# Performance work log

Measured on AMD Instinct MI355X. Metric: run time of the kernel, lower is better.

## Reference

```python
import jax, jax.numpy as jnp
import numpy as np

B, S, H = 2, 2048, 1024
NH, HD = 16, 64
WIN = 256
EPS = 1e-5


def _layernorm(x, g, b):
    # normalize over last dim (head_dim)
    m = jnp.mean(x, axis=-1, keepdims=True)
    v = jnp.mean((x - m) ** 2, axis=-1, keepdims=True)
    return (x - m) * jax.lax.rsqrt(v + EPS) * g + b


def setup_inputs() -> dict:
    key = jax.random.key(0)
    ks = jax.random.split(key, 6)
    scale = 1.0 / np.sqrt(2.0 * H)  # ~ xavier_uniform with gain 1/sqrt(2)
    inp = {
        "x": jax.random.normal(ks[0], (B, S, H), dtype=jnp.float32),
        "Wq": jax.random.normal(ks[1], (H, H), dtype=jnp.float32) * scale,
        "bq": jnp.zeros((H,), jnp.float32),
        "Wk": jax.random.normal(ks[2], (H, H), dtype=jnp.float32) * scale,
        "bk": jnp.zeros((H,), jnp.float32),
        "Wv": jax.random.normal(ks[3], (H, H), dtype=jnp.float32) * scale,
        "bv": jnp.zeros((H,), jnp.float32),
        "Wo": jax.random.normal(ks[4], (H, H), dtype=jnp.float32) * scale,
        "bo": jnp.zeros((H,), jnp.float32),
        "ln_q_w": jnp.ones((HD,), jnp.float32),
        "ln_q_b": jnp.zeros((HD,), jnp.float32),
        "ln_k_w": jnp.ones((HD,), jnp.float32),
        "ln_k_b": jnp.zeros((HD,), jnp.float32),
    }
    return inp


def reference(x, Wq, bq, Wk, bk, Wv, bv, Wo, bo, ln_q_w, ln_q_b, ln_k_w, ln_k_b):
    b, s, _ = x.shape
    # projections (torch Linear: x @ W.T + b)
    q = (x @ Wq.T + bq).reshape(b, s, NH, HD)
    k = (x @ Wk.T + bk).reshape(b, s, NH, HD)
    v = (x @ Wv.T + bv).reshape(b, s, NH, HD)
    # QK layernorm over head_dim
    q = _layernorm(q, ln_q_w, ln_q_b)
    k = _layernorm(k, ln_k_w, ln_k_b)
    # scores [b, h, s, s]
    scores = jnp.einsum("bqhd,bkhd->bhqk", q, k) / np.sqrt(HD).astype(np.float32)
    i = jnp.arange(s)[:, None]
    j = jnp.arange(s)[None, :]
    mask = (j <= i) & (i - j <= WIN)
    scores = jnp.where(mask[None, None], scores, -jnp.inf)
    probs = jax.nn.softmax(scores, axis=-1)
    out = jnp.einsum("bhqk,bkhd->bqhd", probs, v).reshape(b, s, NH * HD)
    return out @ Wo.T + bo
```

## Files before the change

### kernel.cpp

```cpp
#include <hip/hip_runtime.h>
#include <hip/hip_bf16.h>
#include <cstdint>

typedef __hip_bfloat16 bf16;
typedef __attribute__((ext_vector_type(8))) short s16x8;
typedef __attribute__((ext_vector_type(4))) float f32x4;

#define NB_B 2
#define NB_S 2048
#define NB_H 1024
#define NB_NH 16
#define NB_HD 64
#define NB_WIN 256
#define NTOK 4096

static __device__ __forceinline__ unsigned pack_bf16(float a, float b) {
    bf16 ta = __float2bfloat16(a), tb = __float2bfloat16(b);
    return (unsigned)*(unsigned short*)&ta | ((unsigned)*(unsigned short*)&tb << 16);
}
static __device__ __forceinline__ unsigned short bf16u(float a) {
    bf16 t = __float2bfloat16(a);
    return *(unsigned short*)&t;
}

__global__ void k_castall(const float* __restrict__ x, const float* __restrict__ Wq,
                          const float* __restrict__ Wk, const float* __restrict__ Wv,
                          const float* __restrict__ Wo,
                          bf16* __restrict__ xb, bf16* __restrict__ wqkvb,
                          bf16* __restrict__ wob) {
    int idx = blockIdx.x * blockDim.x + threadIdx.x;
    const float* in; bf16* out; int i;
    if (idx < 1048576)        { in = x;  out = xb;              i = idx * 4; }
    else if (idx < 1310720)   { in = Wq; out = wqkvb;           i = (idx - 1048576) * 4; }
    else if (idx < 1572864)   { in = Wk; out = wqkvb + 1048576; i = (idx - 1310720) * 4; }
    else if (idx < 1835008)   { in = Wv; out = wqkvb + 2097152; i = (idx - 1572864) * 4; }
    else                      { in = Wo; out = wob;             i = (idx - 1835008) * 4; }
    const float4 v = *(const float4*)(in + i);
    ushort4 u;
    u.x = bf16u(v.x); u.y = bf16u(v.y); u.z = bf16u(v.z); u.w = bf16u(v.w);
    *(ushort4*)((unsigned short*)out + i) = u;
}

__global__ __launch_bounds__(256) void k_gemm_qkv(const bf16* __restrict__ A,
                                                  const bf16* __restrict__ Bw,
                                                  const float* __restrict__ bq,
                                                  const float* __restrict__ bk,
                                                  const float* __restrict__ bv,
                                                  const float* __restrict__ lqw,
                                                  const float* __restrict__ lqb,
                                                  const float* __restrict__ lkw,
                                                  const float* __restrict__ lkb,
                                                  bf16* __restrict__ qbuf,
                                                  bf16* __restrict__ kbuf,
                                                  bf16* __restrict__ vtb) {
    const int K = 1024, N = 3072;
    __shared__ bf16 As[128 * 64];
    __shared__ bf16 Bs[128 * 64];
    const int tid = threadIdx.x;
    const int lane = tid & 63;
    const int w = tid >> 6;
    const int wr = w >> 1, wc = w & 1;

    const int orig = blockIdx.y * gridDim.x + blockIdx.x;
    const int wk = (orig & 7) * 96 + (orig >> 3);
    const int m0 = (wk / 24) * 128, n0 = (wk % 24) * 128;

    const int g = lane >> 4, q = lane & 15;

    f32x4 acc[4][4] = {};

    for (int kt = 0; kt < K; kt += 64) {
#pragma unroll
        for (int it = 0; it < 4; ++it) {
            int c = it * 256 + tid;
            int row = c >> 3, pc = c & 7;
            int col = ((pc ^ (row & 7)) << 3);
            const bf16* ga = A + (size_t)(m0 + row) * K + kt + col;
            __builtin_amdgcn_global_load_lds(
                (const __attribute__((address_space(1))) void*)ga,
                (__attribute__((address_space(3))) void*)(As + c * 8), 16, 0, 0);
            const bf16* gb = Bw + (size_t)(n0 + row) * K + kt + col;
            __builtin_amdgcn_global_load_lds(
                (const __attribute__((address_space(1))) void*)gb,
                (__attribute__((address_space(3))) void*)(Bs + c * 8), 16, 0, 0);
        }
        __syncthreads();

#pragma unroll
        for (int kk = 0; kk < 2; ++kk) {
            const int rchunk = (((kk << 2) + g) ^ (q & 7)) << 3;
            s16x8 af[4], bfr[4];
#pragma unroll
            for (int mi = 0; mi < 4; ++mi)
                af[mi] = *(const s16x8*)&As[(wr * 64 + mi * 16 + q) * 64 + rchunk];
#pragma unroll
            for (int ni = 0; ni < 4; ++ni)
                bfr[ni] = *(const s16x8*)&Bs[(wc * 64 + ni * 16 + q) * 64 + rchunk];
#pragma unroll
            for (int mi = 0; mi < 4; ++mi)
#pragma unroll
                for (int ni = 0; ni < 4; ++ni)
                    acc[mi][ni] = __builtin_amdgcn_mfma_f32_16x16x32_bf16(
                        af[mi], bfr[ni], acc[mi][ni], 0, 0, 0);
        }
        __syncthreads();
    }

    const int col0 = n0 + wc * 64;
    const int hh = col0 >> 6;
    const int csub = col0 & 1023;
    const float* bias = (hh < 16) ? bq : (hh < 32) ? bk : bv;

    float bcol[4];
#pragma unroll
    for (int ni = 0; ni < 4; ++ni) bcol[ni] = bias[csub + ni * 16 + q];
#pragma unroll
    for (int mi = 0; mi < 4; ++mi)
#pragma unroll
        for (int ni = 0; ni < 4; ++ni)
#pragma unroll
            for (int r = 0; r < 4; ++r) acc[mi][ni][r] += bcol[ni];

    if (hh < 32) {
        const float* gwa = (hh < 16) ? lqw : lkw;
        const float* gba = (hh < 16) ? lqb : lkb;
        float gam[4], bet[4];
#pragma unroll
        for (int ni = 0; ni < 4; ++ni) {
            gam[ni] = gwa[ni * 16 + q];
            bet[ni] = gba[ni * 16 + q];
        }
        bf16* outp = (hh < 16) ? qbuf : kbuf;
#pragma unroll
        for (int mi = 0; mi < 4; ++mi)
#pragma unroll
            for (int r = 0; r < 4; ++r) {
                float s1 = acc[mi][0][r] + acc[mi][1][r] + acc[mi][2][r] + acc[mi][3][r];
                float s2 = acc[mi][0][r] * acc[mi][0][r] + acc[mi][1][r] * acc[mi][1][r]
                         + acc[mi][2][r] * acc[mi][2][r] + acc[mi][3][r] * acc[mi][3][r];
#pragma unroll
                for (int mm = 1; mm < 16; mm <<= 1) {
                    s1 += __shfl_xor(s1, mm, 64);
                    s2 += __shfl_xor(s2, mm, 64);
                }
                float mean = s1 * (1.f / 64.f);
                float var = s2 * (1.f / 64.f) - mean * mean;
                float rs = rsqrtf(var + 1e-5f);
                int token = m0 + wr * 64 + mi * 16 + g * 4 + r;
#pragma unroll
                for (int ni = 0; ni < 4; ++ni) {
                    float y = (acc[mi][ni][r] - mean) * rs * gam[ni] + bet[ni];
                    outp[(size_t)token * 1024 + csub + ni * 16 + q] = __float2bfloat16(y);
                }
            }
    } else {
        const int b = m0 >> 11;
        const int bh = b * 16 + (csub >> 6);
        const int sbase0 = (m0 & 2047) + wr * 64 + g * 4;
#pragma unroll
        for (int mi = 0; mi < 4; ++mi) {
            const int sb = sbase0 + mi * 16;
#pragma unroll
            for (int ni = 0; ni < 4; ++ni) {
                const int d = ni * 16 + q;
                ushort4 u;
                u.x = bf16u(acc[mi][ni][0]); u.y = bf16u(acc[mi][ni][1]);
                u.z = bf16u(acc[mi][ni][2]); u.w = bf16u(acc[mi][ni][3]);
                *(ushort4*)(vtb + ((size_t)bh * 64 + d) * 2048 + sb) = u;
            }
        }
    }
}

template <int OUT_BF16>
__global__ __launch_bounds__(256) void k_gemm(const bf16* __restrict__ A,
                                              const bf16* __restrict__ Bw,
                                              const float* __restrict__ bias,
                                              void* __restrict__ Cv,
                                              int M, int N, int K,
                                              int nbx, int cpx) {
    __shared__ bf16 As[128 * 64];
    __shared__ bf16 Bs[128 * 64];
    const int tid = threadIdx.x;
    const int lane = tid & 63;
    const int w = tid >> 6;
    const int wr = w >> 1, wc = w & 1;

    const int orig = blockIdx.y * gridDim.x + blockIdx.x;
    const int wk = (orig & 7) * cpx + (orig >> 3);
    const int m0 = (wk / nbx) * 128, n0 = (wk % nbx) * 128;

    const int g = lane >> 4, q = lane & 15;

    f32x4 acc[4][4] = {};

    for (int kt = 0; kt < K; kt += 64) {
#pragma unroll
        for (int it = 0; it < 4; ++it) {
            int c = it * 256 + tid;
            int row = c >> 3, pc = c & 7;
            int col = ((pc ^ (row & 7)) << 3);
            const bf16* ga = A + (size_t)(m0 + row) * K + kt + col;
            __builtin_amdgcn_global_load_lds(
                (const __attribute__((address_space(1))) void*)ga,
                (__attribute__((address_space(3))) void*)(As + c * 8), 16, 0, 0);
            const bf16* gb = Bw + (size_t)(n0 + row) * K + kt + col;
            __builtin_amdgcn_global_load_lds(
                (const __attribute__((address_space(1))) void*)gb,
                (__attribute__((address_space(3))) void*)(Bs + c * 8), 16, 0, 0);
        }
        __syncthreads();

#pragma unroll
        for (int kk = 0; kk < 2; ++kk) {
            const int rchunk = (((kk << 2) + g) ^ (q & 7)) << 3;
            s16x8 af[4], bfr[4];
#pragma unroll
            for (int mi = 0; mi < 4; ++mi)
                af[mi] = *(const s16x8*)&As[(wr * 64 + mi * 16 + q) * 64 + rchunk];
#pragma unroll
            for (int ni = 0; ni < 4; ++ni)
                bfr[ni] = *(const s16x8*)&Bs[(wc * 64 + ni * 16 + q) * 64 + rchunk];
#pragma unroll
            for (int mi = 0; mi < 4; ++mi)
#pragma unroll
                for (int ni = 0; ni < 4; ++ni)
                    acc[mi][ni] = __builtin_amdgcn_mfma_f32_16x16x32_bf16(
                        af[mi], bfr[ni], acc[mi][ni], 0, 0, 0);
        }
        __syncthreads();
    }

#pragma unroll
    for (int mi = 0; mi < 4; ++mi)
#pragma unroll
        for (int ni = 0; ni < 4; ++ni) {
            int colg = n0 + wc * 64 + ni * 16 + q;
            float bcol = bias[colg];
#pragma unroll
            for (int r = 0; r < 4; ++r) {
                int rowg = m0 + wr * 64 + mi * 16 + g * 4 + r;
                float vlu = acc[mi][ni][r] + bcol;
                if (OUT_BF16)
                    ((bf16*)Cv)[(size_t)rowg * N + colg] = __float2bfloat16(vlu);
                else
                    ((float*)Cv)[(size_t)rowg * N + colg] = vlu;
            }
        }
}

__global__ __launch_bounds__(256) void k_attn(const bf16* __restrict__ qb,
                                              const bf16* __restrict__ kb,
                                              const bf16* __restrict__ vt,
                                              bf16* __restrict__ att) {
    __shared__ bf16 Ks[2][32 * 64];
    __shared__ bf16 Vs[2][64 * 32];

    const int orig = blockIdx.y * gridDim.x + blockIdx.x;
    const int wk = (orig & 7) * 128 + (orig >> 3);
    const int q0 = (wk & 31) * 64;
    const int bh = wk >> 5;

    const int b = bh >> 4, h = bh & 15;
    const int tid = threadIdx.x;
    const int w = tid >> 6;
    const int lane = tid & 63;
    const int g = lane >> 4, qi = lane & 15;
    const int qw0 = q0 + w * 16;
    const int iq = qw0 + qi;

    const size_t qbase = ((size_t)(b * 2048 + iq)) * 1024 + h * 64 + g * 8;
    s16x8 bq0 = *(const s16x8*)(qb + qbase);
    s16x8 bq1 = *(const s16x8*)(qb + qbase + 32);

    f32x4 o[4] = {};
    float lp = 0.f;

    int jmin = q0 - NB_WIN; if (jmin < 0) jmin = 0;
    const int c0 = jmin >> 5;
    const int c1 = (q0 + 63) >> 5;

    const int krow = tid >> 3, kpc = tid & 7;
    const int kcol = ((kpc ^ (krow & 7)) << 3);
    const int vrow = tid >> 2, vpc = tid & 3;
    const int vcol = ((vpc ^ (vrow & 3)) << 3);
    const bf16* kbase = kb + ((size_t)(b * 2048 + krow)) * 1024 + h * 64 + kcol;
    const bf16* vbase = vt + ((size_t)bh * 64 + vrow) * 2048 + vcol;

    __builtin_amdgcn_global_load_lds(
        (const __attribute__((address_space(1))) void*)(kbase + (size_t)(c0 * 32) * 1024),
        (__attribute__((address_space(3))) void*)(&Ks[0][tid * 8]), 16, 0, 0);
    __builtin_amdgcn_global_load_lds(
        (const __attribute__((address_space(1))) void*)(vbase + c0 * 32),
        (__attribute__((address_space(3))) void*)(&Vs[0][tid * 8]), 16, 0, 0);
    __syncthreads();

    int buf = 0;
    for (int c = c0; c <= c1; ++c) {
        const int ks = c * 32;
        if (c < c1) {
            const int ksn = ks + 32;
            __builtin_amdgcn_global_load_lds(
                (const __attribute__((address_space(1))) void*)(kbase + (size_t)ksn * 1024),
                (__attribute__((address_space(3))) void*)(&Ks[buf ^ 1][tid * 8]), 16, 0, 0);
            __builtin_amdgcn_global_load_lds(
                (const __attribute__((address_space(1))) void*)(vbase + ksn),
                (__attribute__((address_space(3))) void*)(&Vs[buf ^ 1][tid * 8]), 16, 0, 0);
        }

        if (ks + 31 >= qw0 - NB_WIN && ks <= qw0 + 15) {
            const int ch0 = ((g ^ (qi & 7)) << 3);
            const bf16* kr0 = &Ks[buf][qi * 64];
            const bf16* kr1 = &Ks[buf][(16 + qi) * 64];
            s16x8 a00 = *(const s16x8*)(kr0 + ch0);
            s16x8 a01 = *(const s16x8*)(kr0 + (ch0 ^ 32));
            s16x8 a10 = *(const s16x8*)(kr1 + ch0);
            s16x8 a11 = *(const s16x8*)(kr1 + (ch0 ^ 32));

            f32x4 s0 = {}, s1 = {};
            s0 = __builtin_amdgcn_mfma_f32_16x16x32_bf16(a00, bq0, s0, 0, 0, 0);
            s0 = __builtin_amdgcn_mfma_f32_16x16x32_bf16(a01, bq1, s0, 0, 0, 0);
            s1 = __builtin_amdgcn_mfma_f32_16x16x32_bf16(a10, bq0, s1, 0, 0, 0);
            s1 = __builtin_amdgcn_mfma_f32_16x16x32_bf16(a11, bq1, s1, 0, 0, 0);

            float p0[4], p1[4];
#pragma unroll
            for (int r = 0; r < 4; ++r) {
                int j0 = ks + 4 * g + r, j1 = j0 + 16;
                p0[r] = ((unsigned)(iq - j0) <= (unsigned)NB_WIN)
                            ? __expf(s0[r] * 0.125f - 8.f) : 0.f;
                p1[r] = ((unsigned)(iq - j1) <= (unsigned)NB_WIN)
                            ? __expf(s1[r] * 0.125f - 8.f) : 0.f;
                lp += p0[r] + p1[r];
            }
            unsigned P0 = pack_bf16(p0[0], p0[1]), P1 = pack_bf16(p0[2], p0[3]);
            unsigned Q0 = pack_bf16(p1[0], p1[1]), Q1 = pack_bf16(p1[2], p1[3]);

            const int srcA = qi + (g & 1) * 32;
            const int srcB = srcA + 16;
            unsigned tP0a = __shfl((int)P0, srcA, 64), tQ0a = __shfl((int)Q0, srcA, 64);
            unsigned tP1a = __shfl((int)P1, srcA, 64), tQ1a = __shfl((int)Q1, srcA, 64);
            unsigned tP0b = __shfl((int)P0, srcB, 64), tQ0b = __shfl((int)Q0, srcB, 64);
            unsigned tP1b = __shfl((int)P1, srcB, 64), tQ1b = __shfl((int)Q1, srcB, 64);
            union { s16x8 v; unsigned u[4]; } pa;
            pa.u[0] = (g < 2) ? tP0a : tQ0a;
            pa.u[1] = (g < 2) ? tP1a : tQ1a;
            pa.u[2] = (g < 2) ? tP0b : tQ0b;
            pa.u[3] = (g < 2) ? tP1b : tQ1b;

            const int chv = ((g ^ (qi & 3)) << 3);
#pragma unroll
            for (int db = 0; db < 4; ++db) {
                s16x8 bv = *(const s16x8*)&Vs[buf][(db * 16 + qi) * 32 + chv];
                o[db] = __builtin_amdgcn_mfma_f32_16x16x32_bf16(pa.v, bv, o[db], 0, 0, 0);
            }
        }

        __syncthreads();
        buf ^= 1;
    }

    float l2 = lp + __shfl_xor(lp, 16, 64);
    float lf = l2 + __shfl_xor(l2, 32, 64);
    float lr[4];
#pragma unroll
    for (int r = 0; r < 4; ++r) lr[r] = __shfl(lf, 4 * g + r, 64);

#pragma unroll
    for (int db = 0; db < 4; ++db)
#pragma unroll
        for (int r = 0; r < 4; ++r) {
            float vlu = o[db][r] / lr[r];
            att[((size_t)(b * 2048 + qw0 + 4 * g + r)) * 1024 + h * 64 + db * 16 + qi] =
                __float2bfloat16(vlu);
        }
}

extern "C" void kernel_launch(void* const* d_in, const int* in_sizes, int n_in,
                              void* d_out, int out_size, void* d_ws, size_t ws_size,
                              hipStream_t stream) {
    const float* x   = (const float*)d_in[0];
    const float* Wq  = (const float*)d_in[1];
    const float* bq  = (const float*)d_in[2];
    const float* Wk  = (const float*)d_in[3];
    const float* bk  = (const float*)d_in[4];
    const float* Wv  = (const float*)d_in[5];
    const float* bv  = (const float*)d_in[6];
    const float* Wo  = (const float*)d_in[7];
    const float* bo  = (const float*)d_in[8];
    const float* lqw = (const float*)d_in[9];
    const float* lqb = (const float*)d_in[10];
    const float* lkw = (const float*)d_in[11];
    const float* lkb = (const float*)d_in[12];

    char* ws = (char*)d_ws;
    bf16* xb    = (bf16*)(ws + 0);
    bf16* wqkvb = (bf16*)(ws + 8388608);
    bf16* wob   = (bf16*)(ws + 14680064);
    bf16* qbuf  = (bf16*)(ws + 16777216);
    bf16* kbuf  = (bf16*)(ws + 25165824);
    bf16* vtb   = (bf16*)(ws + 33554432);
    bf16* attb  = (bf16*)(ws + 41943040);

    k_castall<<<8192, 256, 0, stream>>>(x, Wq, Wk, Wv, Wo, xb, wqkvb, wob);

    k_gemm_qkv<<<dim3(24, 32), 256, 0, stream>>>(xb, wqkvb, bq, bk, bv,
                                                 lqw, lqb, lkw, lkb,
                                                 qbuf, kbuf, vtb);

    k_attn<<<dim3(32, 32), 256, 0, stream>>>(qbuf, kbuf, vtb, attb);

    k_gemm<0><<<dim3(8, 32), 256, 0, stream>>>(attb, wob, bo, d_out, NTOK, NB_H, NB_H, 8, 32);
}
```

Measured before the change: 101.7 us.

## Double-buffer LDS tiles in QKV and output GEMMs with MFMA priority boost

Both GEMM kernels now use two LDS buffers for the A and B tiles, so the global-to-LDS loads for the next K-slice are issued before the MFMAs on the current slice run. This hides global load latency and halves the barriers per K-step. The MFMA blocks are wrapped in s_setprio to favour the math waves, and the output GEMM is specialised with hard-coded sizes. LDS per block doubles to 64 KB, which may reduce occupancy.

```diff
diff --git a/kernel.cpp b/kernel.cpp
--- a/kernel.cpp
+++ b/kernel.cpp
@@ -41,8 +41,48 @@
     *(ushort4*)((unsigned short*)out + i) = u;
 }
 
-__global__ __launch_bounds__(256) void k_gemm_qkv(const bf16* __restrict__ A,
-                                                  const bf16* __restrict__ Bw,
+#define G_STAGE(AD, BD, KT)                                                          \
+    do {                                                                             \
+        _Pragma("unroll")                                                            \
+        for (int it_ = 0; it_ < 4; ++it_) {                                          \
+            int c_ = it_ * 256 + tid;                                                \
+            int row_ = c_ >> 3, pc_ = c_ & 7;                                        \
+            int col_ = ((pc_ ^ (row_ & 7)) << 3);                                    \
+            __builtin_amdgcn_global_load_lds(                                        \
+                (const __attribute__((address_space(1))) void*)(Ap + (size_t)(m0 + row_) * 1024 + (KT) + col_), \
+                (__attribute__((address_space(3))) void*)((AD) + c_ * 8), 16, 0, 0); \
+            __builtin_amdgcn_global_load_lds(                                        \
+                (const __attribute__((address_space(1))) void*)(Bp + (size_t)(n0 + row_) * 1024 + (KT) + col_), \
+                (__attribute__((address_space(3))) void*)((BD) + c_ * 8), 16, 0, 0); \
+        }                                                                            \
+        __builtin_amdgcn_sched_barrier(0);                                           \
+    } while (0)
+
+#define G_COMPUTE(AS, BS)                                                            \
+    do {                                                                             \
+        _Pragma("unroll")                                                            \
+        for (int kk_ = 0; kk_ < 2; ++kk_) {                                          \
+            const int rchunk_ = (((kk_ << 2) + g) ^ (q & 7)) << 3;                   \
+            s16x8 af_[4], bf_[4];                                                    \
+            _Pragma("unroll")                                                        \
+            for (int mi_ = 0; mi_ < 4; ++mi_)                                        \
+                af_[mi_] = *(const s16x8*)&(AS)[(wr * 64 + mi_ * 16 + q) * 64 + rchunk_]; \
+            _Pragma("unroll")                                                        \
+            for (int ni_ = 0; ni_ < 4; ++ni_)                                        \
+                bf_[ni_] = *(const s16x8*)&(BS)[(wc * 64 + ni_ * 16 + q) * 64 + rchunk_]; \
+            __builtin_amdgcn_s_setprio(1);                                           \
+            _Pragma("unroll")                                                        \
+            for (int mi_ = 0; mi_ < 4; ++mi_)                                        \
+                _Pragma("unroll")                                                    \
+                for (int ni_ = 0; ni_ < 4; ++ni_)                                    \
+                    acc[mi_][ni_] = __builtin_amdgcn_mfma_f32_16x16x32_bf16(         \
+                        af_[mi_], bf_[ni_], acc[mi_][ni_], 0, 0, 0);                 \
+            __builtin_amdgcn_s_setprio(0);                                           \
+        }                                                                            \
+    } while (0)
+
+__global__ __launch_bounds__(256) void k_gemm_qkv(const bf16* __restrict__ Ap,
+                                                  const bf16* __restrict__ Bp,
                                                   const float* __restrict__ bq,
                                                   const float* __restrict__ bk,
                                                   const float* __restrict__ bv,
@@ -53,9 +93,8 @@
                                                   bf16* __restrict__ qbuf,
                                                   bf16* __restrict__ kbuf,
                                                   bf16* __restrict__ vtb) {
-    const int K = 1024, N = 3072;
-    __shared__ bf16 As[128 * 64];
-    __shared__ bf16 Bs[128 * 64];
+    __shared__ bf16 As0[128 * 64], As1[128 * 64];
+    __shared__ bf16 Bs0[128 * 64], Bs1[128 * 64];
     const int tid = threadIdx.x;
     const int lane = tid & 63;
     const int w = tid >> 6;
@@ -69,40 +108,15 @@
 
     f32x4 acc[4][4] = {};
 
-    for (int kt = 0; kt < K; kt += 64) {
-#pragma unroll
-        for (int it = 0; it < 4; ++it) {
-            int c = it * 256 + tid;
-            int row = c >> 3, pc = c & 7;
-            int col = ((pc ^ (row & 7)) << 3);
-            const bf16* ga = A + (size_t)(m0 + row) * K + kt + col;
-            __builtin_amdgcn_global_load_lds(
-                (const __attribute__((address_space(1))) void*)ga,
-                (__attribute__((address_space(3))) void*)(As + c * 8), 16, 0, 0);
-            const bf16* gb = Bw + (size_t)(n0 + row) * K + kt + col;
-            __builtin_amdgcn_global_load_lds(
-                (const __attribute__((address_space(1))) void*)gb,
-                (__attribute__((address_space(3))) void*)(Bs + c * 8), 16, 0, 0);
-        }
-        __syncthreads();
-
-#pragma unroll
-        for (int kk = 0; kk < 2; ++kk) {
-            const int rchunk = (((kk << 2) + g) ^ (q & 7)) << 3;
-            s16x8 af[4], bfr[4];
-#pragma unroll
-            for (int mi = 0; mi < 4; ++mi)
-                af[mi] = *(const s16x8*)&As[(wr * 64 + mi * 16 + q) * 64 + rchunk];
-#pragma unroll
-            for (int ni = 0; ni < 4; ++ni)
-                bfr[ni] = *(const s16x8*)&Bs[(wc * 64 + ni * 16 + q) * 64 + rchunk];
-#pragma unroll
-            for (int mi = 0; mi < 4; ++mi)
-#pragma unroll
-                for (int ni = 0; ni < 4; ++ni)
-                    acc[mi][ni] = __builtin_amdgcn_mfma_f32_16x16x32_bf16(
-                        af[mi], bfr[ni], acc[mi][ni], 0, 0, 0);
-        }
+    G_STAGE(As0, Bs0, 0);
+    __syncthreads();
+#pragma unroll 2
+    for (int kt = 0; kt < 1024; kt += 128) {
+        G_STAGE(As1, Bs1, kt + 64);
+        G_COMPUTE(As0, Bs0);
+        __syncthreads();
+        if (kt + 128 < 1024) G_STAGE(As0, Bs0, kt + 128);
+        G_COMPUTE(As1, Bs1);
         __syncthreads();
     }
 
@@ -172,62 +186,34 @@
     }
 }
 
-template <int OUT_BF16>
-__global__ __launch_bounds__(256) void k_gemm(const bf16* __restrict__ A,
-                                              const bf16* __restrict__ Bw,
-                                              const float* __restrict__ bias,
-                                              void* __restrict__ Cv,
-                                              int M, int N, int K,
-                                              int nbx, int cpx) {
-    __shared__ bf16 As[128 * 64];
-    __shared__ bf16 Bs[128 * 64];
+__global__ __launch_bounds__(256) void k_gemm_out(const bf16* __restrict__ Ap,
+                                                  const bf16* __restrict__ Bp,
+                                                  const float* __restrict__ bias,
+                                                  float* __restrict__ Cv) {
+    __shared__ bf16 As0[128 * 64], As1[128 * 64];
+    __shared__ bf16 Bs0[128 * 64], Bs1[128 * 64];
     const int tid = threadIdx.x;
     const int lane = tid & 63;
     const int w = tid >> 6;
     const int wr = w >> 1, wc = w & 1;
 
     const int orig = blockIdx.y * gridDim.x + blockIdx.x;
-    const int wk = (orig & 7) * cpx + (orig >> 3);
-    const int m0 = (wk / nbx) * 128, n0 = (wk % nbx) * 128;
+    const int wk = (orig & 7) * 32 + (orig >> 3);
+    const int m0 = (wk / 8) * 128, n0 = (wk % 8) * 128;
 
     const int g = lane >> 4, q = lane & 15;
 
     f32x4 acc[4][4] = {};
 
-    for (int kt = 0; kt < K; kt += 64) {
-#pragma unroll
-        for (int it = 0; it < 4; ++it) {
-            int c = it * 256 + tid;
-            int row = c >> 3, pc = c & 7;
-            int col = ((pc ^ (row & 7)) << 3);
-            const bf16* ga = A + (size_t)(m0 + row) * K + kt + col;
-            __builtin_amdgcn_global_load_lds(
-                (const __attribute__((address_space(1))) void*)ga,
-                (__attribute__((address_space(3))) void*)(As + c * 8), 16, 0, 0);
-            const bf16* gb = Bw + (size_t)(n0 + row) * K + kt + col;
-            __builtin_amdgcn_global_load_lds(
-                (const __attribute__((address_space(1))) void*)gb,
-                (__attribute__((address_space(3))) void*)(Bs + c * 8), 16, 0, 0);
-        }
-        __syncthreads();
-
-#pragma unroll
-        for (int kk = 0; kk < 2; ++kk) {
-            const int rchunk = (((kk << 2) + g) ^ (q & 7)) << 3;
-            s16x8 af[4], bfr[4];
-#pragma unroll
-            for (int mi = 0; mi < 4; ++mi)
-                af[mi] = *(const s16x8*)&As[(wr * 64 + mi * 16 + q) * 64 + rchunk];
-#pragma unroll
-            for (int ni = 0; ni < 4; ++ni)
-                bfr[ni] = *(const s16x8*)&Bs[(wc * 64 + ni * 16 + q) * 64 + rchunk];
-#pragma unroll
-            for (int mi = 0; mi < 4; ++mi)
-#pragma unroll
-                for (int ni = 0; ni < 4; ++ni)
-                    acc[mi][ni] = __builtin_amdgcn_mfma_f32_16x16x32_bf16(
-                        af[mi], bfr[ni], acc[mi][ni], 0, 0, 0);
-        }
+    G_STAGE(As0, Bs0, 0);
+    __syncthreads();
+#pragma unroll 2
+    for (int kt = 0; kt < 1024; kt += 128) {
+        G_STAGE(As1, Bs1, kt + 64);
+        G_COMPUTE(As0, Bs0);
+        __syncthreads();
+        if (kt + 128 < 1024) G_STAGE(As0, Bs0, kt + 128);
+        G_COMPUTE(As1, Bs1);
         __syncthreads();
     }
 
@@ -240,14 +226,13 @@
 #pragma unroll
             for (int r = 0; r < 4; ++r) {
                 int rowg = m0 + wr * 64 + mi * 16 + g * 4 + r;
-                float vlu = acc[mi][ni][r] + bcol;
-                if (OUT_BF16)
-                    ((bf16*)Cv)[(size_t)rowg * N + colg] = __float2bfloat16(vlu);
-                else
-                    ((float*)Cv)[(size_t)rowg * N + colg] = vlu;
-            }
-        }
-}
+                Cv[(size_t)rowg * 1024 + colg] = acc[mi][ni][r] + bcol;
+            }
+        }
+}
+
+#undef G_STAGE
+#undef G_COMPUTE
 
 __global__ __launch_bounds__(256) void k_attn(const bf16* __restrict__ qb,
                                               const bf16* __restrict__ kb,
@@ -410,5 +395,5 @@
 
     k_attn<<<dim3(32, 32), 256, 0, stream>>>(qbuf, kbuf, vtb, attb);
 
-    k_gemm<0><<<dim3(8, 32), 256, 0, stream>>>(attb, wob, bo, d_out, NTOK, NB_H, NB_H, 8, 32);
-}
+    k_gemm_out<<<dim3(8, 32), 256, 0, stream>>>(attb, wob, bo, (float*)d_out);
+}
```

Measured after the change: 91.35 us. 1.11x faster.
